# Kernel optimization log

Measured on AMD Instinct MI355X. Metric: run time of the kernel, lower is better.

Reference implementation:

```python
import jax, jax.numpy as jnp
import numpy as np
import math

D_MODEL = 1024
NUM_HEADS = 16
ROPE_THETA = 10000.0
BATCH = 4
SEQ = 2048


def apply_rope(x, pos, theta=ROPE_THETA):
    # x: (b, h, s, d_k), pos: (s,) int positions
    d = x.shape[-1]
    inv_freq = theta ** (-jnp.arange(0, d, 2, dtype=jnp.float32) / d)  # (d/2,)
    ang = pos.astype(jnp.float32)[:, None] * inv_freq                  # (s, d/2)
    cos, sin = jnp.cos(ang), jnp.sin(ang)
    x1, x2 = x[..., 0::2], x[..., 1::2]
    # interleave rotated pairs back to last dim
    out = jnp.stack([x1 * cos - x2 * sin, x1 * sin + x2 * cos], axis=-1)
    return out.reshape(x.shape)


def setup_inputs() -> dict:
    key = jax.random.key(0)
    ks = jax.random.split(key, 5)
    scale = 1.0 / math.sqrt(D_MODEL)
    return {
        "x": jax.random.normal(ks[0], (BATCH, SEQ, D_MODEL), dtype=jnp.float32),
        "token_positions": jnp.arange(SEQ, dtype=jnp.int64 if jax.config.jax_enable_x64 else jnp.int32),
        "Wq": jax.random.normal(ks[1], (D_MODEL, D_MODEL), dtype=jnp.float32) * scale,
        "Wk": jax.random.normal(ks[2], (D_MODEL, D_MODEL), dtype=jnp.float32) * scale,
        "Wv": jax.random.normal(ks[3], (D_MODEL, D_MODEL), dtype=jnp.float32) * scale,
        "Wo": jax.random.normal(ks[4], (D_MODEL, D_MODEL), dtype=jnp.float32) * scale,
    }


def reference(x, token_positions, Wq, Wk, Wv, Wo):
    b, s, d_model = x.shape
    h = NUM_HEADS
    d_k = d_model // h

    def proj_split(W):
        # Linear: y = x @ W.T (W is (out,in)); then split heads -> (b, h, s, d_k)
        y = jnp.einsum('bsi,oi->bso', x, W)
        return y.reshape(b, s, h, d_k).transpose(0, 2, 1, 3)

    q = apply_rope(proj_split(Wq), token_positions)
    k = apply_rope(proj_split(Wk), token_positions)
    v = proj_split(Wv)

    scores = jnp.einsum('bhqd,bhkd->bhqk', q, k) / jnp.asarray(math.sqrt(d_k), x.dtype)
    causal = jnp.tril(jnp.ones((s, s), dtype=bool))  # (s, s) keep lower triangle
    scores = jnp.where(causal, scores, jnp.asarray(-jnp.inf, scores.dtype))
    attn = jax.nn.softmax(scores, axis=-1)
    out = jnp.einsum('bhqk,bhkd->bhqd', attn, v)
    out = out.transpose(0, 2, 1, 3).reshape(b, s, d_model)
    return jnp.einsum('bsi,oi->bso', out, Wo)
```

## Files before the change

### kernel.cpp

```cpp
#include <hip/hip_runtime.h>
#include <cstdint>
#include <cstddef>


typedef __attribute__((ext_vector_type(8))) short bf16x8;
typedef __attribute__((ext_vector_type(4))) float f32x4;

#define LOG2E 1.4426950408889634f

__device__ __forceinline__ unsigned short f2bf(float f) {
  unsigned int u = __builtin_bit_cast(unsigned int, f);
  unsigned int r = (u + 0x7FFFu + ((u >> 16) & 1u)) >> 16;
  return (unsigned short)r;
}
__device__ __forceinline__ float bf2f(unsigned short h) {
  return __builtin_bit_cast(float, (unsigned int)h << 16);
}
__device__ __forceinline__ unsigned int packbf2(float a, float b) {
  return (unsigned int)f2bf(a) | ((unsigned int)f2bf(b) << 16);
}
__device__ __forceinline__ unsigned int cvtpk(float lo, float hi) {
  unsigned int r;
  asm("v_cvt_pk_bf16_f32 %0, %1, %2" : "=v"(r) : "v"(lo), "v"(hi));
  return r;
}
__device__ __forceinline__ int swz(int idx) {
  return idx ^ (((idx >> 6) & 7) << 3);
}

__global__ __launch_bounds__(256) void cvt_kernel(const float* __restrict__ in,
                                                  unsigned short* __restrict__ out,
                                                  int n8) {
  int i = blockIdx.x * 256 + threadIdx.x;
  if (i < n8) {
    float4 u0 = ((const float4*)in)[i * 2];
    float4 u1 = ((const float4*)in)[i * 2 + 1];
    uint4 v = {packbf2(u0.x, u0.y), packbf2(u0.z, u0.w),
               packbf2(u1.x, u1.y), packbf2(u1.z, u1.w)};
    ((uint4*)out)[i] = v;
  }
}
__global__ __launch_bounds__(256) void cvt_w3(const float* __restrict__ w0,
                                              const float* __restrict__ w1,
                                              const float* __restrict__ w2,
                                              unsigned short* __restrict__ dst) {
  const float* src = blockIdx.y == 0 ? w0 : (blockIdx.y == 1 ? w1 : w2);
  unsigned short* d = dst + (size_t)blockIdx.y * 1024 * 1024;
  int i = blockIdx.x * 256 + threadIdx.x;
  float4 u0 = ((const float4*)src)[i * 2];
  float4 u1 = ((const float4*)src)[i * 2 + 1];
  uint4 v = {packbf2(u0.x, u0.y), packbf2(u0.z, u0.w),
             packbf2(u1.x, u1.y), packbf2(u1.z, u1.w)};
  ((uint4*)d)[i] = v;
}

__global__ __launch_bounds__(256) void gemm_qkv(const unsigned short* __restrict__ Xb,
                                                const unsigned short* __restrict__ Wb3,
                                                unsigned short* __restrict__ Qb,
                                                unsigned short* __restrict__ Kb,
                                                unsigned short* __restrict__ Vtb) {
  __shared__ alignas(16) unsigned short As[128 * 64];
  __shared__ alignas(16) unsigned short Bs[128 * 64];
  const int t = threadIdx.x;
  const int lane = t & 63;
  const int w = t >> 6;
  const int wr = w >> 1, wc = w & 1;
  const int fr = lane & 15, fq = lane >> 4;
  const int m0 = blockIdx.x * 128;
  const int sel = blockIdx.y >> 3;
  const int n0 = (blockIdx.y & 7) * 128;
  const unsigned short* Wp = Wb3 + (size_t)sel * 1024 * 1024;
  const int K = 1024;

  const f32x4 zero = {0.f, 0.f, 0.f, 0.f};
  f32x4 acc[4][4];
#pragma unroll
  for (int m = 0; m < 4; ++m)
#pragma unroll
    for (int n = 0; n < 4; ++n) acc[m][n] = zero;

  for (int k0 = 0; k0 < K; k0 += 64) {
#pragma unroll
    for (int cc = 0; cc < 4; ++cc) {
      int c = w * 4 + cc;
      int flat = c * 512 + lane * 8;
      int row = flat >> 6, col = flat & 63;
      __builtin_amdgcn_global_load_lds(
          (const __attribute__((address_space(1))) void*)(Xb + (size_t)(m0 + row) * K + (k0 + col)),
          (__attribute__((address_space(3))) void*)&As[c * 512], 16, 0, 0);
      __builtin_amdgcn_global_load_lds(
          (const __attribute__((address_space(1))) void*)(Wp + (size_t)(n0 + row) * K + (k0 + col)),
          (__attribute__((address_space(3))) void*)&Bs[c * 512], 16, 0, 0);
    }
    __syncthreads();
#pragma unroll
    for (int kk = 0; kk < 2; ++kk) {
      bf16x8 a[4], b[4];
#pragma unroll
      for (int m = 0; m < 4; ++m)
        a[m] = *(const bf16x8*)&As[(wr * 64 + m * 16 + fr) * 64 + kk * 32 + fq * 8];
#pragma unroll
      for (int n = 0; n < 4; ++n)
        b[n] = *(const bf16x8*)&Bs[(wc * 64 + n * 16 + fr) * 64 + kk * 32 + fq * 8];
#pragma unroll
      for (int m = 0; m < 4; ++m)
#pragma unroll
        for (int n = 0; n < 4; ++n)
          acc[m][n] = __builtin_amdgcn_mfma_f32_16x16x32_bf16(a[m], b[n], acc[m][n], 0, 0, 0);
    }
    __syncthreads();
  }

#pragma unroll
  for (int m = 0; m < 4; ++m)
#pragma unroll
    for (int n = 0; n < 4; ++n) {
      int row = m0 + wr * 64 + m * 16 + fq * 4;
      int col = n0 + wc * 64 + n * 16 + fr;
      if (sel < 2) {
        unsigned short* Cp = sel ? Kb : Qb;
#pragma unroll
        for (int j = 0; j < 4; ++j)
          Cp[(size_t)(row + j) * 1024 + col] = f2bf(acc[m][n][j]);
      } else {
        int b = row >> 11, s = row & 2047;
        int h = col >> 6, d = col & 63;
        ushort4 v4 = {f2bf(acc[m][n][0]), f2bf(acc[m][n][1]),
                      f2bf(acc[m][n][2]), f2bf(acc[m][n][3])};
        *(ushort4*)&Vtb[(((size_t)b * 16 + h) * 64 + d) * 2048 + s] = v4;
      }
    }
}

__global__ __launch_bounds__(256) void rope_kernel(unsigned short* __restrict__ Q,
                                                   unsigned short* __restrict__ Kb,
                                                   const int* __restrict__ tp) {
  int idx = blockIdx.x * 256 + threadIdx.x;
  unsigned short* ptr = blockIdx.y ? Kb : Q;
  const float scale = blockIdx.y ? 1.0f : 0.125f * LOG2E;
  int flat8 = idx * 8;
  int r = flat8 >> 10;
  int colbase = flat8 & 1023;
  int ibase = (colbase & 63) >> 1;
  int s = r & 2047;
  float pos = (float)tp[s];
  const float cexp = -13.287712379549449f / 32.0f;

  uint4 v = *(const uint4*)&ptr[flat8];
  unsigned int* vp = (unsigned int*)&v;
  uint4 o;
  unsigned int* op = (unsigned int*)&o;
#pragma unroll
  for (int p = 0; p < 4; ++p) {
    float inv = exp2f((float)(ibase + p) * cexp);
    float ang = pos * inv;
    float sn, cs;
    sincosf(ang, &sn, &cs);
    float x1 = bf2f((unsigned short)(vp[p] & 0xFFFFu));
    float x2 = bf2f((unsigned short)(vp[p] >> 16));
    op[p] = packbf2((x1 * cs - x2 * sn) * scale, (x1 * sn + x2 * cs) * scale);
  }
  *(uint4*)&ptr[flat8] = o;
}

__global__ __launch_bounds__(256) void attn_kernel(const unsigned short* __restrict__ Q,
                                                   const unsigned short* __restrict__ K,
                                                   const unsigned short* __restrict__ Vt_g,
                                                   unsigned short* __restrict__ O) {
  __shared__ alignas(16) unsigned short Ks[64 * 64];
  __shared__ alignas(16) unsigned short Vt[64 * 64];
  const int t = threadIdx.x;
  const int lane = t & 63, w = t >> 6;
  const int fr = lane & 15, fq = lane >> 4;
  const int gblk = (blockIdx.x & 7) * 64 + (blockIdx.x >> 3);
  const int pairidx = gblk & 7;
  const int hb = gblk >> 3;
  const int h = hb & 15, b = hb >> 4;
  const size_t base = ((size_t)b * 2048) * 1024 + (size_t)h * 64;
  const size_t vbase = ((size_t)b * 16 + h) * 64 * 2048;
  const f32x4 zero = {0.f, 0.f, 0.f, 0.f};

  const int sflat = t * 8;
  const int srow0 = sflat >> 6, scol = sflat & 63;

  for (int pass = 0; pass < 2; ++pass) {
    const int qt = pass ? (15 - pairidx) : pairidx;
    const int q0 = qt * 128;
    const int wq = q0 + w * 32;
    const int kvend = q0 + 128;

    bf16x8 qf[2][2];
#pragma unroll
    for (int g = 0; g < 2; ++g)
#pragma unroll
      for (int kk = 0; kk < 2; ++kk)
        qf[g][kk] = *(const bf16x8*)&Q[base + (size_t)(q0 + w * 32 + g * 16 + fr) * 1024 + kk * 32 + fq * 8];

    float m_[2] = {-INFINITY, -INFINITY};
    float l_[2] = {0.f, 0.f};
    f32x4 oaccT[2][4];
#pragma unroll
    for (int g = 0; g < 2; ++g)
#pragma unroll
      for (int n = 0; n < 4; ++n) oaccT[g][n] = zero;

    uint4 kr[2], vr[2];
#pragma unroll
    for (int it = 0; it < 2; ++it) {
      int row = srow0 + it * 32;
      kr[it] = *(const uint4*)&K[base + (size_t)row * 1024 + scol];
      vr[it] = *(const uint4*)&Vt_g[vbase + (size_t)row * 2048 + scol];
    }

    for (int kv0 = 0; kv0 < kvend; kv0 += 64) {
      __syncthreads();
#pragma unroll
      for (int it = 0; it < 2; ++it) {
        int flat = sflat + it * 2048;
        *(uint4*)&Ks[swz(flat)] = kr[it];
        *(uint4*)&Vt[swz(flat)] = vr[it];
      }
      __syncthreads();
      if (kv0 + 64 < kvend) {
#pragma unroll
        for (int it = 0; it < 2; ++it) {
          int row = srow0 + it * 32;
          kr[it] = *(const uint4*)&K[base + (size_t)(kv0 + 64 + row) * 1024 + scol];
          vr[it] = *(const uint4*)&Vt_g[vbase + (size_t)row * 2048 + kv0 + 64 + scol];
        }
      }

      if (kv0 <= wq + 31) {
        bf16x8 kf[2][4];
#pragma unroll
        for (int kk = 0; kk < 2; ++kk)
#pragma unroll
          for (int n = 0; n < 4; ++n)
            kf[kk][n] = *(const bf16x8*)&Ks[swz((n * 16 + fr) * 64 + kk * 32 + fq * 8)];

#pragma unroll
        for (int g = 0; g < 2; ++g) {
          if (kv0 > wq + g * 16 + 15) continue;
          f32x4 sa[4];
#pragma unroll
          for (int n = 0; n < 4; ++n) sa[n] = zero;
#pragma unroll
          for (int kk = 0; kk < 2; ++kk)
#pragma unroll
            for (int n = 0; n < 4; ++n)
              sa[n] = __builtin_amdgcn_mfma_f32_16x16x32_bf16(kf[kk][n], qf[g][kk], sa[n], 0, 0, 0);

          const int dd = kv0 - wq - g * 16;
          if (dd > -63) {
#pragma unroll
            for (int n = 0; n < 4; ++n)
#pragma unroll
              for (int j = 0; j < 4; ++j)
                if (n * 16 + fq * 4 + j + dd > fr) sa[n][j] = -3.0e38f;
          }

          float pmax = -3.0e38f;
#pragma unroll
          for (int n = 0; n < 4; ++n)
#pragma unroll
            for (int j = 0; j < 4; ++j) pmax = fmaxf(pmax, sa[n][j]);
          pmax = fmaxf(pmax, __shfl_xor(pmax, 16));
          pmax = fmaxf(pmax, __shfl_xor(pmax, 32));
          if (!__all(pmax <= m_[g])) {
            float mn = fmaxf(m_[g], pmax);
            float alpha = exp2f(m_[g] - mn);
            m_[g] = mn;
            l_[g] *= alpha;
#pragma unroll
            for (int n = 0; n < 4; ++n)
#pragma unroll
              for (int j = 0; j < 4; ++j) oaccT[g][n][j] *= alpha;
          }
          float ps = 0.f;
#pragma unroll
          for (int n = 0; n < 4; ++n)
#pragma unroll
            for (int j = 0; j < 4; ++j) {
              float e = exp2f(sa[n][j] - m_[g]);
              sa[n][j] = e;
              ps += e;
            }
          ps += __shfl_xor(ps, 16);
          ps += __shfl_xor(ps, 32);
          l_[g] += ps;

          unsigned R[4][2], F[4][2];
#pragma unroll
          for (int n = 0; n < 4; ++n)
#pragma unroll
            for (int pp = 0; pp < 2; ++pp)
              R[n][pp] = cvtpk(sa[n][2 * pp], sa[n][2 * pp + 1]);
#pragma unroll
          for (int pp = 0; pp < 2; ++pp) {
            unsigned t0 = (fq < 2) ? R[1][pp] : R[0][pp];
            unsigned t1 = (fq < 2) ? R[3][pp] : R[2][pp];
            t0 = (unsigned)__shfl_xor((int)t0, 32);
            t1 = (unsigned)__shfl_xor((int)t1, 32);
            unsigned G0 = (fq < 2) ? R[0][pp] : t0;
            unsigned G1 = (fq < 2) ? t0 : R[1][pp];
            unsigned G2 = (fq < 2) ? R[2][pp] : t1;
            unsigned G3 = (fq < 2) ? t1 : R[3][pp];
            unsigned u0 = ((fq & 1) == 0) ? G1 : G0;
            unsigned u1 = ((fq & 1) == 0) ? G3 : G2;
            u0 = (unsigned)__shfl_xor((int)u0, 16);
            u1 = (unsigned)__shfl_xor((int)u1, 16);
            F[0][pp] = ((fq & 1) == 0) ? G0 : u0;
            F[1][pp] = ((fq & 1) == 0) ? u0 : G1;
            F[2][pp] = ((fq & 1) == 0) ? G2 : u1;
            F[3][pp] = ((fq & 1) == 0) ? u1 : G3;
          }
          union U8 { unsigned u[4]; bf16x8 v; };
          U8 pb0, pb1;
          pb0.u[0] = F[0][0]; pb0.u[1] = F[0][1]; pb0.u[2] = F[1][0]; pb0.u[3] = F[1][1];
          pb1.u[0] = F[2][0]; pb1.u[1] = F[2][1]; pb1.u[2] = F[3][0]; pb1.u[3] = F[3][1];

#pragma unroll
          for (int n = 0; n < 4; ++n) {
            bf16x8 vf0 = *(const bf16x8*)&Vt[swz((n * 16 + fr) * 64 + 0 * 32 + fq * 8)];
            oaccT[g][n] = __builtin_amdgcn_mfma_f32_16x16x32_bf16(vf0, pb0.v, oaccT[g][n], 0, 0, 0);
            bf16x8 vf1 = *(const bf16x8*)&Vt[swz((n * 16 + fr) * 64 + 1 * 32 + fq * 8)];
            oaccT[g][n] = __builtin_amdgcn_mfma_f32_16x16x32_bf16(vf1, pb1.v, oaccT[g][n], 0, 0, 0);
          }
        }
      }
    }

#pragma unroll
    for (int g = 0; g < 2; ++g) {
      float rl = 1.0f / l_[g];
#pragma unroll
      for (int n = 0; n < 4; ++n) {
        ushort4 v4 = {f2bf(oaccT[g][n][0] * rl), f2bf(oaccT[g][n][1] * rl),
                      f2bf(oaccT[g][n][2] * rl), f2bf(oaccT[g][n][3] * rl)};
        *(ushort4*)&O[base + (size_t)(q0 + w * 32 + g * 16 + fr) * 1024 + n * 16 + fq * 4] = v4;
      }
    }
  }
}

__global__ __launch_bounds__(256) void gemm_out_bf(const unsigned short* __restrict__ Ap,
                                                   const unsigned short* __restrict__ Wp,
                                                   float* __restrict__ Cp) {
  __shared__ alignas(16) unsigned short As[128 * 64];
  __shared__ alignas(16) unsigned short Bs[128 * 64];
  const int t = threadIdx.x;
  const int lane = t & 63;
  const int w = t >> 6;
  const int wr = w >> 1, wc = w & 1;
  const int fr = lane & 15, fq = lane >> 4;
  const int m0 = blockIdx.x * 128, n0 = blockIdx.y * 128;
  const int K = 1024, N = 1024;

  const f32x4 zero = {0.f, 0.f, 0.f, 0.f};
  f32x4 acc[4][4];
#pragma unroll
  for (int m = 0; m < 4; ++m)
#pragma unroll
    for (int n = 0; n < 4; ++n) acc[m][n] = zero;

  for (int k0 = 0; k0 < K; k0 += 64) {
#pragma unroll
    for (int cc = 0; cc < 4; ++cc) {
      int c = w * 4 + cc;
      int flat = c * 512 + lane * 8;
      int row = flat >> 6, col = flat & 63;
      __builtin_amdgcn_global_load_lds(
          (const __attribute__((address_space(1))) void*)(Ap + (size_t)(m0 + row) * K + (k0 + col)),
          (__attribute__((address_space(3))) void*)&As[c * 512], 16, 0, 0);
      __builtin_amdgcn_global_load_lds(
          (const __attribute__((address_space(1))) void*)(Wp + (size_t)(n0 + row) * K + (k0 + col)),
          (__attribute__((address_space(3))) void*)&Bs[c * 512], 16, 0, 0);
    }
    __syncthreads();
#pragma unroll
    for (int kk = 0; kk < 2; ++kk) {
      bf16x8 a[4], b[4];
#pragma unroll
      for (int m = 0; m < 4; ++m)
        a[m] = *(const bf16x8*)&As[(wr * 64 + m * 16 + fr) * 64 + kk * 32 + fq * 8];
#pragma unroll
      for (int n = 0; n < 4; ++n)
        b[n] = *(const bf16x8*)&Bs[(wc * 64 + n * 16 + fr) * 64 + kk * 32 + fq * 8];
#pragma unroll
      for (int m = 0; m < 4; ++m)
#pragma unroll
        for (int n = 0; n < 4; ++n)
          acc[m][n] = __builtin_amdgcn_mfma_f32_16x16x32_bf16(a[m], b[n], acc[m][n], 0, 0, 0);
    }
    __syncthreads();
  }

#pragma unroll
  for (int m = 0; m < 4; ++m)
#pragma unroll
    for (int n = 0; n < 4; ++n) {
      int row = m0 + wr * 64 + m * 16 + fq * 4;
      int col = n0 + wc * 64 + n * 16 + fr;
#pragma unroll
      for (int j = 0; j < 4; ++j)
        Cp[(size_t)(row + j) * N + col] = acc[m][n][j];
    }
}

extern "C" void kernel_launch(void* const* d_in, const int* in_sizes, int n_in,
                              void* d_out, int out_size, void* d_ws, size_t ws_size,
                              hipStream_t stream) {
  const float* x  = (const float*)d_in[0];
  const int* tp   = (const int*)d_in[1];
  const float* Wq = (const float*)d_in[2];
  const float* Wk = (const float*)d_in[3];
  const float* Wv = (const float*)d_in[4];
  const float* Wo = (const float*)d_in[5];
  float* out = (float*)d_out;

  const size_t MAT = (size_t)8192 * 1024;
  unsigned short* Qb  = (unsigned short*)d_ws;
  unsigned short* Kb  = Qb + MAT;
  unsigned short* Vtb = Kb + MAT;
  unsigned short* Xb  = Vtb + MAT;
  unsigned short* Ob  = Xb;
  unsigned short* Wb3 = (unsigned short*)d_out;
  unsigned short* WoB = Qb;

  cvt_kernel<<<4096, 256, 0, stream>>>(x, Xb, 8192 * 1024 / 8);
  cvt_w3<<<dim3(512, 3), 256, 0, stream>>>(Wq, Wk, Wv, Wb3);
  gemm_qkv<<<dim3(64, 24), 256, 0, stream>>>(Xb, Wb3, Qb, Kb, Vtb);
  rope_kernel<<<dim3(4096, 2), 256, 0, stream>>>(Qb, Kb, tp);
  attn_kernel<<<512, 256, 0, stream>>>(Qb, Kb, Vtb, Ob);
  cvt_kernel<<<512, 256, 0, stream>>>(Wo, WoB, 1024 * 1024 / 8);
  gemm_out_bf<<<dim3(64, 8), 256, 0, stream>>>(Ob, WoB, out);
}
```

Baseline: 344.8 us.

## Fuse RoPE and Q scaling into QKV GEMM epilogue with LDS-staged stores

Removes the separate RoPE kernel and applies the rotation and Q scaling inside the QKV GEMM epilogue. Rotation pairs come from neighbouring lanes via shuffle. Results are staged through a swizzled shared buffer so Q/K are written with coalesced 16-byte stores instead of scattered 2-byte stores. This avoids a full read and write of Q and K plus one launch, at the cost of sincos work and an extra sync in the GEMM epilogue.

```diff
diff --git a/kernel.cpp b/kernel.cpp
--- a/kernel.cpp
+++ b/kernel.cpp
@@ -26,6 +26,9 @@
 }
 __device__ __forceinline__ int swz(int idx) {
   return idx ^ (((idx >> 6) & 7) << 3);
+}
+__device__ __forceinline__ int swz128(int idx) {
+  return idx ^ (((idx >> 7) & 7) << 3);
 }
 
 __global__ __launch_bounds__(256) void cvt_kernel(const float* __restrict__ in,
@@ -56,11 +59,13 @@
 
 __global__ __launch_bounds__(256) void gemm_qkv(const unsigned short* __restrict__ Xb,
                                                 const unsigned short* __restrict__ Wb3,
+                                                const int* __restrict__ tp,
                                                 unsigned short* __restrict__ Qb,
                                                 unsigned short* __restrict__ Kb,
                                                 unsigned short* __restrict__ Vtb) {
-  __shared__ alignas(16) unsigned short As[128 * 64];
-  __shared__ alignas(16) unsigned short Bs[128 * 64];
+  __shared__ alignas(16) unsigned short sh[128 * 128];
+  unsigned short* As = sh;
+  unsigned short* Bs = sh + 128 * 64;
   const int t = threadIdx.x;
   const int lane = t & 63;
   const int w = t >> 6;
@@ -111,56 +116,56 @@
     __syncthreads();
   }
 
-#pragma unroll
-  for (int m = 0; m < 4; ++m)
+  if (sel < 2) {
+    unsigned short* Cp = sel ? Kb : Qb;
+    const float qscale = sel ? 1.0f : 0.125f * LOG2E;
+    const float cexp = -13.287712379549449f / 32.0f;
+    const int col_lo = wc * 64;
 #pragma unroll
     for (int n = 0; n < 4; ++n) {
-      int row = m0 + wr * 64 + m * 16 + fq * 4;
-      int col = n0 + wc * 64 + n * 16 + fr;
-      if (sel < 2) {
-        unsigned short* Cp = sel ? Kb : Qb;
-#pragma unroll
-        for (int j = 0; j < 4; ++j)
-          Cp[(size_t)(row + j) * 1024 + col] = f2bf(acc[m][n][j]);
-      } else {
+      int lc = col_lo + n * 16 + fr;
+      int i = ((n0 + lc) & 63) >> 1;
+      float inv = exp2f((float)i * cexp);
+      int lr0 = wr * 64 + fq * 4;
+#pragma unroll
+      for (int m = 0; m < 4; ++m) {
+        int lr = lr0 + m * 16;
+        int s = (m0 + lr) & 2047;
+        int4 tpv = *(const int4*)&tp[s];
+        const int* tpp = (const int*)&tpv;
+#pragma unroll
+        for (int j = 0; j < 4; ++j) {
+          float own = acc[m][n][j];
+          float part = __shfl_xor(own, 1);
+          float ang = (float)tpp[j] * inv;
+          float sn, cs;
+          sincosf(ang, &sn, &cs);
+          float o = (fr & 1) ? (part * sn + own * cs) : (own * cs - part * sn);
+          sh[swz128((lr + j) * 128 + lc)] = f2bf(o * qscale);
+        }
+      }
+    }
+    __syncthreads();
+#pragma unroll
+    for (int c = 0; c < 8; ++c) {
+      int flat = c * 2048 + t * 8;
+      int r = flat >> 7, col = flat & 127;
+      *(uint4*)&Cp[(size_t)(m0 + r) * 1024 + n0 + col] = *(const uint4*)&sh[swz128(flat)];
+    }
+  } else {
+#pragma unroll
+    for (int m = 0; m < 4; ++m)
+#pragma unroll
+      for (int n = 0; n < 4; ++n) {
+        int row = m0 + wr * 64 + m * 16 + fq * 4;
+        int col = n0 + wc * 64 + n * 16 + fr;
         int b = row >> 11, s = row & 2047;
         int h = col >> 6, d = col & 63;
         ushort4 v4 = {f2bf(acc[m][n][0]), f2bf(acc[m][n][1]),
                       f2bf(acc[m][n][2]), f2bf(acc[m][n][3])};
         *(ushort4*)&Vtb[(((size_t)b * 16 + h) * 64 + d) * 2048 + s] = v4;
       }
-    }
-}
-
-__global__ __launch_bounds__(256) void rope_kernel(unsigned short* __restrict__ Q,
-                                                   unsigned short* __restrict__ Kb,
-                                                   const int* __restrict__ tp) {
-  int idx = blockIdx.x * 256 + threadIdx.x;
-  unsigned short* ptr = blockIdx.y ? Kb : Q;
-  const float scale = blockIdx.y ? 1.0f : 0.125f * LOG2E;
-  int flat8 = idx * 8;
-  int r = flat8 >> 10;
-  int colbase = flat8 & 1023;
-  int ibase = (colbase & 63) >> 1;
-  int s = r & 2047;
-  float pos = (float)tp[s];
-  const float cexp = -13.287712379549449f / 32.0f;
-
-  uint4 v = *(const uint4*)&ptr[flat8];
-  unsigned int* vp = (unsigned int*)&v;
-  uint4 o;
-  unsigned int* op = (unsigned int*)&o;
-#pragma unroll
-  for (int p = 0; p < 4; ++p) {
-    float inv = exp2f((float)(ibase + p) * cexp);
-    float ang = pos * inv;
-    float sn, cs;
-    sincosf(ang, &sn, &cs);
-    float x1 = bf2f((unsigned short)(vp[p] & 0xFFFFu));
-    float x2 = bf2f((unsigned short)(vp[p] >> 16));
-    op[p] = packbf2((x1 * cs - x2 * sn) * scale, (x1 * sn + x2 * cs) * scale);
   }
-  *(uint4*)&ptr[flat8] = o;
 }
 
 __global__ __launch_bounds__(256) void attn_kernel(const unsigned short* __restrict__ Q,
@@ -429,8 +434,7 @@
 
   cvt_kernel<<<4096, 256, 0, stream>>>(x, Xb, 8192 * 1024 / 8);
   cvt_w3<<<dim3(512, 3), 256, 0, stream>>>(Wq, Wk, Wv, Wb3);
-  gemm_qkv<<<dim3(64, 24), 256, 0, stream>>>(Xb, Wb3, Qb, Kb, Vtb);
-  rope_kernel<<<dim3(4096, 2), 256, 0, stream>>>(Qb, Kb, tp);
+  gemm_qkv<<<dim3(64, 24), 256, 0, stream>>>(Xb, Wb3, tp, Qb, Kb, Vtb);
   attn_kernel<<<512, 256, 0, stream>>>(Qb, Kb, Vtb, Ob);
   cvt_kernel<<<512, 256, 0, stream>>>(Wo, WoB, 1024 * 1024 / 8);
   gemm_out_bf<<<dim3(64, 8), 256, 0, stream>>>(Ob, WoB, out);
```

After: 514.4 us. +49.2%, slower.
